# Performance work log

Hardware: AMD Instinct MI355X
Metric: run time of the kernel (lower is better)

Reference implementation:

```python
import jax, jax.numpy as jnp
import numpy as np

D_MODEL = 512
NUM_HEADS = 8
HEAD_DIM = D_MODEL // NUM_HEADS
BATCH = 4
SEQ = 2048
ROPE_BASE = 10000.0


def rope_cos_sin(seq_len, head_dim):
    inv_freq = 1.0 / (ROPE_BASE ** (jnp.arange(0, head_dim, 2, dtype=jnp.float32) / head_dim))
    t = jnp.arange(seq_len, dtype=jnp.float32)
    freqs = jnp.outer(t, inv_freq)              # (S, head_dim/2)
    emb = jnp.concatenate([freqs, freqs], axis=-1)  # (S, head_dim)
    return jnp.cos(emb), jnp.sin(emb)


def apply_rope(x, cos, sin):
    # x: (..., S, head_dim); cos/sin: (S, head_dim)
    x1 = x[..., ::2]
    x2 = x[..., 1::2]
    ch = cos[..., ::2]
    sh = sin[..., ::2]
    r1 = x1 * ch - x2 * sh
    r2 = x1 * sh + x2 * ch
    return jnp.stack([r1, r2], axis=-1).reshape(x.shape)


def setup_inputs() -> dict:
    key = jax.random.key(0)
    ks = jax.random.split(key, 12)
    x = jax.random.normal(ks[0], (BATCH, SEQ, D_MODEL), dtype=jnp.float32)
    variate_ids = jnp.sort(jax.random.randint(ks[1], (BATCH, SEQ), 0, 8), axis=-1).astype(jnp.int64)
    mask = jnp.ones((BATCH, SEQ), dtype=jnp.float32)
    s = 1.0 / np.sqrt(D_MODEL)
    Wq = jax.random.normal(ks[2], (D_MODEL, D_MODEL), dtype=jnp.float32) * s
    bq = jnp.zeros((D_MODEL,), dtype=jnp.float32)
    Wk = jax.random.normal(ks[3], (D_MODEL, D_MODEL), dtype=jnp.float32) * s
    bk = jnp.zeros((D_MODEL,), dtype=jnp.float32)
    Wv = jax.random.normal(ks[4], (D_MODEL, D_MODEL), dtype=jnp.float32) * s
    bv = jnp.zeros((D_MODEL,), dtype=jnp.float32)
    Wo = jax.random.normal(ks[5], (D_MODEL, D_MODEL), dtype=jnp.float32) * s
    bo = jnp.zeros((D_MODEL,), dtype=jnp.float32)
    u_same = jax.random.normal(ks[6], (NUM_HEADS,), dtype=jnp.float32) * 0.1
    u_cross = jax.random.normal(ks[7], (NUM_HEADS,), dtype=jnp.float32) * 0.1
    return dict(x=x, variate_ids=variate_ids, mask=mask, Wq=Wq, bq=bq, Wk=Wk, bk=bk,
                Wv=Wv, bv=bv, Wo=Wo, bo=bo, u_same=u_same, u_cross=u_cross)


def reference(x, variate_ids, mask, Wq, bq, Wk, bk, Wv, bv, Wo, bo, u_same, u_cross):
    B, S, D = x.shape
    H, Hd = NUM_HEADS, HEAD_DIM
    scale = 1.0 / np.sqrt(Hd)

    def proj(W, b):
        return (x @ W.T + b).reshape(B, S, H, Hd).transpose(0, 2, 1, 3)  # (B,H,S,Hd)

    q = proj(Wq, bq)
    k = proj(Wk, bk)
    v = proj(Wv, bv)

    cos, sin = rope_cos_sin(S, Hd)
    q = apply_rope(q, cos, sin)
    k = apply_rope(k, cos, sin)

    scores = jnp.einsum('bhid,bhjd->bhij', q, k) * scale  # (B,H,S,S)
    same = (variate_ids[:, :, None] == variate_ids[:, None, :]).astype(jnp.float32)  # (B,S,S)
    bias = same[:, None] * u_same[None, :, None, None] + (1.0 - same)[:, None] * u_cross[None, :, None, None]
    scores = scores + bias
    scores = scores + (1.0 - mask[:, None, None, :]) * -1e9
    probs = jax.nn.softmax(scores, axis=-1)
    out = jnp.einsum('bhij,bhjd->bhid', probs, v)  # (B,H,S,Hd)
    out = out.transpose(0, 2, 1, 3).reshape(B, S, D)
    return out @ Wo.T + bo
```

## Files before the change

kernel.cpp:

```cpp
#include <hip/hip_runtime.h>
#include <hip/hip_bf16.h>

#define BATCH   4
#define SEQ     2048
#define DMODEL  512
#define NHEADS  8
#define HEADDIM 64
#define MTOT    (BATCH*SEQ)
#define NX      (MTOT*DMODEL)
#define NW      (DMODEL*DMODEL)
#define QTILE   128
#define KTILE   64
#define NKT     (SEQ/KTILE)

#define LOG2E   1.4426950408889634f
#define SCL2    0.18033688011112042f
#define SHIFT   14.426950408889634f

typedef unsigned short u16;
typedef __bf16 bf16x8 __attribute__((ext_vector_type(8)));
typedef float  f32x4  __attribute__((ext_vector_type(4)));
typedef unsigned short u16x4 __attribute__((ext_vector_type(4)));
typedef unsigned u32x2 __attribute__((ext_vector_type(2)));

#define MFMA(a,b,c) __builtin_amdgcn_mfma_f32_16x16x32_bf16(a,b,c,0,0,0)

__device__ __forceinline__ u16 f2bf(float f) {
    unsigned u = __float_as_uint(f);
    u += 0x7FFFu + ((u >> 16) & 1u);
    return (u16)(u >> 16);
}
__device__ __forceinline__ unsigned pk_bf16(float a, float b) {
    union { __hip_bfloat162 h; unsigned u; } cv;
    cv.h = __float22bfloat162_rn(make_float2(a, b));
    return cv.u;
}
__device__ __forceinline__ float qsum16(float v) {
    v += __shfl_xor(v, 1);
    v += __shfl_xor(v, 2);
    v += __shfl_xor(v, 4);
    v += __shfl_xor(v, 8);
    return v;
}
__device__ __forceinline__ void gll16(const void* g, void* l) {
    __builtin_amdgcn_global_load_lds((const __attribute__((address_space(1))) void*)g,
                                     (__attribute__((address_space(3))) void*)l, 16, 0, 0);
}
__device__ __forceinline__ void gll4(const void* g, void* l) {
    __builtin_amdgcn_global_load_lds((const __attribute__((address_space(1))) void*)g,
                                     (__attribute__((address_space(3))) void*)l, 4, 0, 0);
}

#define NCVT4 ((NX + 4*NW)/4)
__global__ __launch_bounds__(256) void cvt_rope_kernel(
    const float* __restrict__ x,
    const float* __restrict__ wq, const float* __restrict__ wk,
    const float* __restrict__ wv, const float* __restrict__ wo,
    u16* __restrict__ xbf,
    u16* __restrict__ wqbf, u16* __restrict__ wkbf,
    u16* __restrict__ wvbf, u16* __restrict__ wobf,
    float2* __restrict__ cst)
{
    int i4 = blockIdx.x * 256 + threadIdx.x;
    if (i4 < NCVT4) {
        int i = i4 * 4;
        const float* s; u16* d; int o;
        if (i < NX) { s = x; d = xbf; o = i; }
        else {
            int j = i - NX;
            int r = j >> 18;
            o = j & (NW - 1);
            s = (r == 0) ? wq : (r == 1) ? wk : (r == 2) ? wv : wo;
            d = (r == 0) ? wqbf : (r == 1) ? wkbf : (r == 2) ? wvbf : wobf;
        }
        float4 v = *(const float4*)(s + o);
        u16x4 u = { f2bf(v.x), f2bf(v.y), f2bf(v.z), f2bf(v.w) };
        *(u16x4*)(d + o) = u;
    } else {
        int r = i4 - NCVT4;
        if (r < SEQ * 32 / 4) {
            int idx = r * 4;
            int s  = idx >> 5;
            int p0 = idx & 31;
#pragma unroll
            for (int t = 0; t < 4; ++t) {
                int p = p0 + t;
                float inv = __expf(-0.5756462732485115f * (float)(p & 15));
                float ang = (float)s * inv;
                cst[idx + t] = make_float2(cosf(ang), sinf(ang));
            }
        }
    }
}

#define TP 136
__global__ __launch_bounds__(256) void qkv_kernel(
    const u16* __restrict__ x,
    const u16* __restrict__ Wq, const float* __restrict__ bq,
    const u16* __restrict__ Wk, const float* __restrict__ bk,
    const u16* __restrict__ Wv, const float* __restrict__ bv,
    const float* __restrict__ cstf,
    u16* __restrict__ qws, u16* __restrict__ kws, u16* __restrict__ vtws)
{
    __shared__ alignas(16) u16 smem[128 * TP];
    u16* As = smem;
    u16* Bs = smem + 8192;

    const int m0 = blockIdx.x * 128;
    const int n0 = blockIdx.y * 128;
    const int tid  = threadIdx.x;
    const int w    = tid >> 6;
    const int lane = tid & 63;
    const int quad = lane >> 4;
    const int l16  = lane & 15;
    const int wm = w & 1, wn = w >> 1;

    const int sec = n0 >> 9;
    const int oc0 = n0 & 511;
    const u16*   Wm = (sec == 0) ? Wq : (sec == 1 ? Wk : Wv);
    const float* bb = (sec == 0) ? bq : (sec == 1 ? bk : bv);

    const int xb = (sec < 2) ? wn : wm;
    const int wb = (sec < 2) ? wm : wn;

    f32x4 acc[4][4] = {};

    for (int kb = 0; kb < 8; ++kb) {
#pragma unroll
        for (int it = 0; it < 4; ++it) {
            const int s   = it * 256 + tid;
            const int row = s >> 3;
            const int cb  = s & 7;
            const int gcol = kb * 64 + (((cb ^ (row & 7))) << 3);
            gll16(x  + (m0  + row) * 512 + gcol, &As[s * 8]);
            gll16(Wm + (oc0 + row) * 512 + gcol, &Bs[s * 8]);
        }
        __syncthreads();

#pragma unroll
        for (int ks = 0; ks < 2; ++ks) {
            bf16x8 xf[4], wf[4];
#pragma unroll
            for (int t = 0; t < 4; ++t) {
                const int xrow = xb * 64 + t * 16 + l16;
                const int wrow = wb * 64 + t * 16 + l16;
                xf[t] = *(const bf16x8*)&As[xrow * 64 + (((ks * 4 + quad) ^ (xrow & 7)) << 3)];
                wf[t] = *(const bf16x8*)&Bs[wrow * 64 + (((ks * 4 + quad) ^ (wrow & 7)) << 3)];
            }
            if (sec < 2) {
#pragma unroll
                for (int tm = 0; tm < 4; ++tm)
#pragma unroll
                    for (int tn = 0; tn < 4; ++tn)
                        acc[tm][tn] = MFMA(wf[tm], xf[tn], acc[tm][tn]);
            } else {
#pragma unroll
                for (int tm = 0; tm < 4; ++tm)
#pragma unroll
                    for (int tn = 0; tn < 4; ++tn)
                        acc[tm][tn] = MFMA(xf[tm], wf[tn], acc[tm][tn]);
            }
        }
        __syncthreads();
    }

    if (sec < 2) {
#pragma unroll
        for (int tm = 0; tm < 4; ++tm) {
            const int dls = wm * 64 + tm * 16 + quad * 4;
            const float4 bv4 = *(const float4*)&bb[oc0 + dls];
            const int pbase = ((oc0 + dls) & 63) >> 1;
#pragma unroll
            for (int tn = 0; tn < 4; ++tn) {
                const int sl = wn * 64 + tn * 16 + l16;
                const int sg = (m0 + sl) & 2047;
                const float4 cs = *(const float4*)&cstf[sg * 64 + pbase * 2];
                const float v0 = acc[tm][tn][0] + bv4.x;
                const float v1 = acc[tm][tn][1] + bv4.y;
                const float v2 = acc[tm][tn][2] + bv4.z;
                const float v3 = acc[tm][tn][3] + bv4.w;
                const float r0 = v0 * cs.x - v1 * cs.y;
                const float r1 = v1 * cs.x + v0 * cs.y;
                const float r2 = v2 * cs.z - v3 * cs.w;
                const float r3 = v3 * cs.z + v2 * cs.w;
                u32x2 pv = { pk_bf16(r0, r1), pk_bf16(r2, r3) };
                *(u32x2*)&smem[sl * TP + dls] = pv;
            }
        }
        __syncthreads();
        u16* dst0 = (sec == 0) ? qws : kws;
#pragma unroll
        for (int i = 0; i < 8; ++i) {
            const int c   = i * 256 + tid;
            const int sl  = c >> 4;
            const int d8  = (c & 15) * 8;
            const int gcol = oc0 + d8;
            const int hh  = gcol >> 6;
            const int dh  = gcol & 63;
            const int sgl = m0 + sl;
            const int bi  = sgl >> 11;
            const int s   = sgl & 2047;
            u16* dst = dst0 + (size_t)(bi * NHEADS + hh) * (SEQ * HEADDIM)
                            + (size_t)s * HEADDIM + dh;
            *(bf16x8*)dst = *(const bf16x8*)&smem[sl * TP + d8];
        }
    } else {
#pragma unroll
        for (int tm = 0; tm < 4; ++tm) {
            const int row_l = wm * 64 + tm * 16 + quad * 4;
#pragma unroll
            for (int tn = 0; tn < 4; ++tn) {
                const int col_l = wn * 64 + tn * 16 + l16;
                const float bval = bb[oc0 + col_l];
                u32x2 pv = { pk_bf16(acc[tm][tn][0] + bval, acc[tm][tn][1] + bval),
                             pk_bf16(acc[tm][tn][2] + bval, acc[tm][tn][3] + bval) };
                *(u32x2*)&smem[col_l * TP + row_l] = pv;
            }
        }
        __syncthreads();
        const int bi  = m0 >> 11;
        const int sgb = m0 & 2047;
#pragma unroll
        for (int i = 0; i < 8; ++i) {
            const int c    = i * 256 + tid;
            const int col  = c >> 4;
            const int sc8  = (c & 15) * 8;
            const int gcol = oc0 + col;
            const int hh   = gcol >> 6;
            const int d    = gcol & 63;
            u16* dst = vtws + (size_t)(bi * NHEADS + hh) * (SEQ * HEADDIM)
                            + (size_t)d * SEQ + sgb + sc8;
            *(bf16x8*)dst = *(const bf16x8*)&smem[col * TP + sc8];
        }
    }
}

__global__ __launch_bounds__(512, 4) void attn_kernel(
    const u16* __restrict__ qws, const u16* __restrict__ kws,
    const u16* __restrict__ vtl,
    const int* __restrict__ vids, const float* __restrict__ mask,
    const float* __restrict__ u_same, const float* __restrict__ u_cross,
    u16* __restrict__ attn)
{
    __shared__ alignas(16) u16 kbuf[2][KTILE * 64];
    __shared__ alignas(16) u16 vbuf[2][KTILE * 64];
    __shared__ alignas(16) u16 pls[8][16][72];
    __shared__ int   bid[2][KTILE];
    __shared__ float bmk[2][KTILE];

    const int bh = blockIdx.y;
    const int b  = bh >> 3;
    const int h  = bh & 7;
    const int q0 = blockIdx.x * QTILE;

    const int tid  = threadIdx.x;
    const int w    = tid >> 6;
    const int lane = tid & 63;
    const int quad = lane >> 4;
    const int l16  = lane & 15;

    const float us2 = u_same[h]  * LOG2E;
    const float uc2 = u_cross[h] * LOG2E;
    const size_t tb = (size_t)bh * (SEQ * HEADDIM);

    const int qr = q0 + w * 16 + l16;
    const bf16x8 aq0 = *(const bf16x8*)(qws + tb + qr * HEADDIM + quad * 8);
    const bf16x8 aq1 = *(const bf16x8*)(qws + tb + qr * HEADDIM + 32 + quad * 8);

    int vq[4];
#pragma unroll
    for (int r = 0; r < 4; ++r)
        vq[r] = vids[b * SEQ + q0 + w * 16 + quad * 4 + r];

    float li[4] = {0.f, 0.f, 0.f, 0.f};
    f32x4 o[4] = {};

    const int srow = w * 8 + (lane >> 3);
    const int scb  = lane & 7;
    const int soff = ((scb ^ (srow & 7)) << 3);
    auto stage = [&](int kt, int nb) {
        const int k0 = kt * KTILE;
        gll16(kws + tb + (size_t)(k0 + srow) * HEADDIM + soff, &kbuf[nb][w * 512 + lane * 8]);
        gll16(vtl + tb + (size_t)srow * SEQ + k0 + soff,       &vbuf[nb][w * 512 + lane * 8]);
        if (w == 0) {
            gll4(vids + b * SEQ + k0 + lane, &bid[nb][0]);
            gll4(mask + b * SEQ + k0 + lane, &bmk[nb][0]);
        }
    };

    auto body = [&](const int cur) {
#pragma unroll
        for (int nt = 0; nt < 4; ++nt) {
            const int krow = nt * 16 + l16;
            const int r7   = krow & 7;
            const bf16x8 kb0 = *(const bf16x8*)&kbuf[cur][krow * 64 + ((quad ^ r7) << 3)];
            const bf16x8 kb1 = *(const bf16x8*)&kbuf[cur][krow * 64 + ((quad ^ r7 ^ 4) << 3)];
            f32x4 sc = {};
            sc = MFMA(aq0, kb0, sc);
            sc = MFMA(aq1, kb1, sc);
            const int   kv  = bid[cur][krow];
            const float mdl = fmaf(bmk[cur][krow], 1.4426950408889634e9f,
                                   -1.4426950408889634e9f - SHIFT);
            const float as_ = us2 + mdl;
            const float ac_ = uc2 + mdl;
            float p[4];
#pragma unroll
            for (int r = 0; r < 4; ++r) {
                const float sel = (kv == vq[r]) ? as_ : ac_;
                p[r] = exp2f(fmaf(sc[r], SCL2, sel));
                li[r] += p[r];
            }
            const unsigned p01 = pk_bf16(p[0], p[1]);
            const unsigned p23 = pk_bf16(p[2], p[3]);
            u16* pb = &pls[w][quad * 4][nt * 16 + l16];
            pb[0]       = (u16)p01;  pb[72]      = (u16)(p01 >> 16);
            pb[2 * 72]  = (u16)p23;  pb[3 * 72]  = (u16)(p23 >> 16);
        }

        const bf16x8 ap0 = *(const bf16x8*)&pls[w][l16][quad * 8];
        const bf16x8 ap1 = *(const bf16x8*)&pls[w][l16][32 + quad * 8];

#pragma unroll
        for (int nt = 0; nt < 4; ++nt) {
            const int vrow = nt * 16 + l16;
            const int r7   = vrow & 7;
            const bf16x8 vb0 = *(const bf16x8*)&vbuf[cur][vrow * 64 + ((quad ^ r7) << 3)];
            const bf16x8 vb1 = *(const bf16x8*)&vbuf[cur][vrow * 64 + ((quad ^ r7 ^ 4) << 3)];
            o[nt] = MFMA(ap0, vb0, o[nt]);
            o[nt] = MFMA(ap1, vb1, o[nt]);
        }
    };

    stage(0, 0);
    for (int kt = 0; kt < NKT; kt += 2) {
        __syncthreads();
        stage(kt + 1, 1);
        body(0);
        __syncthreads();
        if (kt + 2 < NKT) stage(kt + 2, 0);
        body(1);
    }

#pragma unroll
    for (int r = 0; r < 4; ++r) {
        const float inv = 1.0f / qsum16(li[r]);
        const int R = q0 + w * 16 + quad * 4 + r;
        const int rb = (b * SEQ + R) * DMODEL + h * HEADDIM;
#pragma unroll
        for (int nt = 0; nt < 4; ++nt)
            attn[rb + nt * 16 + l16] = f2bf(o[nt][r] * inv);
    }
}

__global__ __launch_bounds__(256) void proj_kernel(
    const u16* __restrict__ a, const u16* __restrict__ Wo,
    const float* __restrict__ bo, float* __restrict__ out)
{
    __shared__ alignas(16) u16 psm[132 * 64 * 2];
    u16* As = psm;
    u16* Bs = psm + 8192;
    float* Lp = (float*)psm;

    const int m0 = blockIdx.x * 128;
    const int n0 = blockIdx.y * 128;
    const int tid  = threadIdx.x;
    const int w    = tid >> 6;
    const int lane = tid & 63;
    const int quad = lane >> 4;
    const int l16  = lane & 15;
    const int wm = w & 1, wn = w >> 1;

    f32x4 acc[4][4] = {};

    for (int kb = 0; kb < 8; ++kb) {
#pragma unroll
        for (int it = 0; it < 4; ++it) {
            const int s   = it * 256 + tid;
            const int row = s >> 3;
            const int cb  = s & 7;
            const int gcol = kb * 64 + (((cb ^ (row & 7))) << 3);
            gll16(a  + (m0 + row) * 512 + gcol, &As[s * 8]);
            gll16(Wo + (n0 + row) * 512 + gcol, &Bs[s * 8]);
        }
        __syncthreads();

#pragma unroll
        for (int ks = 0; ks < 2; ++ks) {
            bf16x8 af[4], wf[4];
#pragma unroll
            for (int t = 0; t < 4; ++t) {
                const int arow = wn * 64 + t * 16 + l16;
                const int wrow = wm * 64 + t * 16 + l16;
                af[t] = *(const bf16x8*)&As[arow * 64 + (((ks * 4 + quad) ^ (arow & 7)) << 3)];
                wf[t] = *(const bf16x8*)&Bs[wrow * 64 + (((ks * 4 + quad) ^ (wrow & 7)) << 3)];
            }
#pragma unroll
            for (int tm = 0; tm < 4; ++tm)
#pragma unroll
                for (int tn = 0; tn < 4; ++tn)
                    acc[tm][tn] = MFMA(wf[tm], af[tn], acc[tm][tn]);
        }
        __syncthreads();
    }

#pragma unroll
    for (int hph = 0; hph < 2; ++hph) {
        if (wn == hph) {
#pragma unroll
            for (int tm = 0; tm < 4; ++tm) {
                const int dls = wm * 64 + tm * 16 + quad * 4;
                const float4 bv4 = *(const float4*)&bo[n0 + dls];
#pragma unroll
                for (int tn = 0; tn < 4; ++tn) {
                    const int s2 = tn * 16 + l16;
                    float4 v = { acc[tm][tn][0] + bv4.x, acc[tm][tn][1] + bv4.y,
                                 acc[tm][tn][2] + bv4.z, acc[tm][tn][3] + bv4.w };
                    *(float4*)&Lp[s2 * 132 + dls] = v;
                }
            }
        }
        __syncthreads();
#pragma unroll
        for (int i = 0; i < 8; ++i) {
            const int c  = i * 256 + tid;
            const int s2 = c >> 5;
            const int dq = (c & 31) * 4;
            float4 v = *(const float4*)&Lp[s2 * 132 + dq];
            *(float4*)&out[(size_t)(m0 + hph * 64 + s2) * 512 + n0 + dq] = v;
        }
        __syncthreads();
    }
}

extern "C" void kernel_launch(void* const* d_in, const int* in_sizes, int n_in,
                              void* d_out, int out_size, void* d_ws, size_t ws_size,
                              hipStream_t stream) {
    const float* x    = (const float*)d_in[0];
    const int*   vids = (const int*)d_in[1];
    const float* mask = (const float*)d_in[2];
    const float* Wq = (const float*)d_in[3];
    const float* bq = (const float*)d_in[4];
    const float* Wk = (const float*)d_in[5];
    const float* bk = (const float*)d_in[6];
    const float* Wv = (const float*)d_in[7];
    const float* bv = (const float*)d_in[8];
    const float* Wo = (const float*)d_in[9];
    const float* bo = (const float*)d_in[10];
    const float* usame  = (const float*)d_in[11];
    const float* ucross = (const float*)d_in[12];
    float* out = (float*)d_out;

    u16* xbf  = (u16*)d_ws;
    u16* wqbf = xbf + NX;
    u16* wkbf = wqbf + NW;
    u16* wvbf = wkbf + NW;
    u16* wobf = wvbf + NW;
    float2* cst = (float2*)(wobf + NW);
    u16* qws  = (u16*)(cst + SEQ * 32);
    u16* kws  = qws + (size_t)BATCH * NHEADS * SEQ * HEADDIM;
    u16* vtws = kws + (size_t)BATCH * NHEADS * SEQ * HEADDIM;
    u16* attn = xbf;

    cvt_rope_kernel<<<(NCVT4 + SEQ * 32 / 4 + 255) / 256, 256, 0, stream>>>(
        x, Wq, Wk, Wv, Wo, xbf, wqbf, wkbf, wvbf, wobf, cst);

    dim3 g1(MTOT / 128, 3 * DMODEL / 128);
    qkv_kernel<<<g1, 256, 0, stream>>>(xbf, wqbf, bq, wkbf, bk, wvbf, bv,
                                       (const float*)cst, qws, kws, vtws);

    dim3 g2(SEQ / QTILE, BATCH * NHEADS);
    attn_kernel<<<g2, 512, 0, stream>>>(qws, kws, vtws, vids, mask,
                                        usame, ucross, attn);

    dim3 g3(MTOT / 128, DMODEL / 128);
    proj_kernel<<<g3, 256, 0, stream>>>(attn, wobf, bo, out);
}
```

Before: 205.6 us.

## Split attention KV range across two wave groups and reduce partials in LDS

The attention kernel now uses a 64-row query tile and splits the key sequence between two groups of four waves. Each group processes half the keys with 32-key tiles, and the partial outputs and row sums are combined through shared memory at the end. This doubles the number of blocks and raises the occupancy hint so more waves can hide latency. It also switches to the hardware exp2 builtin. The cost is an extra LDS reduction pass and smaller MFMA tiles per step, which means more loop overhead per key.

```diff
diff --git a/kernel.cpp b/kernel.cpp
--- a/kernel.cpp
+++ b/kernel.cpp
@@ -9,9 +9,9 @@
 #define MTOT    (BATCH*SEQ)
 #define NX      (MTOT*DMODEL)
 #define NW      (DMODEL*DMODEL)
-#define QTILE   128
-#define KTILE   64
-#define NKT     (SEQ/KTILE)
+#define QTILE   64
+#define KTILE   32
+#define NKT_G   32
 
 #define LOG2E   1.4426950408889634f
 #define SCL2    0.18033688011112042f
@@ -235,18 +235,17 @@
     }
 }
 
-__global__ __launch_bounds__(512, 4) void attn_kernel(
+__global__ __launch_bounds__(512, 6) void attn_kernel(
     const u16* __restrict__ qws, const u16* __restrict__ kws,
     const u16* __restrict__ vtl,
     const int* __restrict__ vids, const float* __restrict__ mask,
     const float* __restrict__ u_same, const float* __restrict__ u_cross,
     u16* __restrict__ attn)
 {
-    __shared__ alignas(16) u16 kbuf[2][KTILE * 64];
-    __shared__ alignas(16) u16 vbuf[2][KTILE * 64];
-    __shared__ alignas(16) u16 pls[8][16][72];
-    __shared__ int   bid[2][KTILE];
-    __shared__ float bmk[2][KTILE];
+    __shared__ alignas(16) u16 smem[21504];
+    __shared__ int   bidm[2][2][KTILE];
+    __shared__ float bmkm[2][2][KTILE];
+    __shared__ float comb_li[QTILE];
 
     const int bh = blockIdx.y;
     const int b  = bh >> 3;
@@ -258,48 +257,62 @@
     const int lane = tid & 63;
     const int quad = lane >> 4;
     const int l16  = lane & 15;
+    const int qw   = w & 3;
+    const int kg   = w >> 2;
+    const int tl   = tid & 255;
 
     const float us2 = u_same[h]  * LOG2E;
     const float uc2 = u_cross[h] * LOG2E;
     const size_t tb = (size_t)bh * (SEQ * HEADDIM);
 
-    const int qr = q0 + w * 16 + l16;
+    const int qr = q0 + qw * 16 + l16;
     const bf16x8 aq0 = *(const bf16x8*)(qws + tb + qr * HEADDIM + quad * 8);
     const bf16x8 aq1 = *(const bf16x8*)(qws + tb + qr * HEADDIM + 32 + quad * 8);
 
     int vq[4];
 #pragma unroll
     for (int r = 0; r < 4; ++r)
-        vq[r] = vids[b * SEQ + q0 + w * 16 + quad * 4 + r];
+        vq[r] = vids[b * SEQ + q0 + qw * 16 + quad * 4 + r];
 
     float li[4] = {0.f, 0.f, 0.f, 0.f};
     f32x4 o[4] = {};
 
-    const int srow = w * 8 + (lane >> 3);
-    const int scb  = lane & 7;
-    const int soff = ((scb ^ (srow & 7)) << 3);
-    auto stage = [&](int kt, int nb) {
-        const int k0 = kt * KTILE;
-        gll16(kws + tb + (size_t)(k0 + srow) * HEADDIM + soff, &kbuf[nb][w * 512 + lane * 8]);
-        gll16(vtl + tb + (size_t)srow * SEQ + k0 + soff,       &vbuf[nb][w * 512 + lane * 8]);
-        if (w == 0) {
-            gll4(vids + b * SEQ + k0 + lane, &bid[nb][0]);
-            gll4(mask + b * SEQ + k0 + lane, &bmk[nb][0]);
+    const int srow  = tl >> 3;
+    const int scb   = tl & 7;
+    const int soff  = ((scb ^ (srow & 7)) << 3);
+    const int vrow  = tl >> 2;
+    const int vcb   = tl & 3;
+    const int soffv = ((vcb ^ (vrow & 3)) << 3);
+    const int kbase = kg * 2 * 2048;
+
+    auto stage = [&](int t, int nb) {
+        const int k0 = (kg * NKT_G + t) * KTILE;
+        gll16(kws + tb + (size_t)(k0 + srow) * HEADDIM + soff,
+              &smem[kbase + nb * 2048 + tl * 8]);
+        gll16(vtl + tb + (size_t)vrow * SEQ + k0 + soffv,
+              &smem[8192 + kbase + nb * 2048 + tl * 8]);
+        if (tl < KTILE) {
+            gll4(vids + b * SEQ + k0 + tl, &bidm[kg][nb][0]);
+            gll4(mask + b * SEQ + k0 + tl, &bmkm[kg][nb][0]);
         }
     };
 
+    u16* const pls = &smem[16384 + w * 640];
+
     auto body = [&](const int cur) {
-#pragma unroll
-        for (int nt = 0; nt < 4; ++nt) {
+        const u16* kb_b = &smem[kbase + cur * 2048];
+        const u16* vb_b = &smem[8192 + kbase + cur * 2048];
+#pragma unroll
+        for (int nt = 0; nt < 2; ++nt) {
             const int krow = nt * 16 + l16;
             const int r7   = krow & 7;
-            const bf16x8 kb0 = *(const bf16x8*)&kbuf[cur][krow * 64 + ((quad ^ r7) << 3)];
-            const bf16x8 kb1 = *(const bf16x8*)&kbuf[cur][krow * 64 + ((quad ^ r7 ^ 4) << 3)];
+            const bf16x8 kb0 = *(const bf16x8*)&kb_b[krow * 64 + ((quad ^ r7) << 3)];
+            const bf16x8 kb1 = *(const bf16x8*)&kb_b[krow * 64 + ((quad ^ r7 ^ 4) << 3)];
             f32x4 sc = {};
             sc = MFMA(aq0, kb0, sc);
             sc = MFMA(aq1, kb1, sc);
-            const int   kv  = bid[cur][krow];
-            const float mdl = fmaf(bmk[cur][krow], 1.4426950408889634e9f,
+            const int   kv  = bidm[kg][cur][krow];
+            const float mdl = fmaf(bmkm[kg][cur][krow], 1.4426950408889634e9f,
                                    -1.4426950408889634e9f - SHIFT);
             const float as_ = us2 + mdl;
             const float ac_ = uc2 + mdl;
@@ -307,48 +320,64 @@
 #pragma unroll
             for (int r = 0; r < 4; ++r) {
                 const float sel = (kv == vq[r]) ? as_ : ac_;
-                p[r] = exp2f(fmaf(sc[r], SCL2, sel));
+                p[r] = __builtin_amdgcn_exp2f(fmaf(sc[r], SCL2, sel));
                 li[r] += p[r];
             }
             const unsigned p01 = pk_bf16(p[0], p[1]);
             const unsigned p23 = pk_bf16(p[2], p[3]);
-            u16* pb = &pls[w][quad * 4][nt * 16 + l16];
-            pb[0]       = (u16)p01;  pb[72]      = (u16)(p01 >> 16);
-            pb[2 * 72]  = (u16)p23;  pb[3 * 72]  = (u16)(p23 >> 16);
-        }
-
-        const bf16x8 ap0 = *(const bf16x8*)&pls[w][l16][quad * 8];
-        const bf16x8 ap1 = *(const bf16x8*)&pls[w][l16][32 + quad * 8];
+            u16* pb = &pls[(quad * 4) * 40 + nt * 16 + l16];
+            pb[0]   = (u16)p01;  pb[40]  = (u16)(p01 >> 16);
+            pb[80]  = (u16)p23;  pb[120] = (u16)(p23 >> 16);
+        }
+
+        const bf16x8 ap0 = *(const bf16x8*)&pls[l16 * 40 + quad * 8];
 
 #pragma unroll
         for (int nt = 0; nt < 4; ++nt) {
-            const int vrow = nt * 16 + l16;
-            const int r7   = vrow & 7;
-            const bf16x8 vb0 = *(const bf16x8*)&vbuf[cur][vrow * 64 + ((quad ^ r7) << 3)];
-            const bf16x8 vb1 = *(const bf16x8*)&vbuf[cur][vrow * 64 + ((quad ^ r7 ^ 4) << 3)];
+            const int vr = nt * 16 + l16;
+            const bf16x8 vb0 = *(const bf16x8*)&vb_b[vr * 32 + ((quad ^ (vr & 3)) << 3)];
             o[nt] = MFMA(ap0, vb0, o[nt]);
-            o[nt] = MFMA(ap1, vb1, o[nt]);
         }
     };
 
     stage(0, 0);
-    for (int kt = 0; kt < NKT; kt += 2) {
-        __syncthreads();
-        stage(kt + 1, 1);
+    for (int t = 0; t < NKT_G; t += 2) {
+        __syncthreads();
+        stage(t + 1, 1);
         body(0);
         __syncthreads();
-        if (kt + 2 < NKT) stage(kt + 2, 0);
+        if (t + 2 < NKT_G) stage(t + 2, 0);
         body(1);
     }
 
-#pragma unroll
-    for (int r = 0; r < 4; ++r) {
-        const float inv = 1.0f / qsum16(li[r]);
-        const int R = q0 + w * 16 + quad * 4 + r;
-        const int rb = (b * SEQ + R) * DMODEL + h * HEADDIM;
+    __syncthreads();
+    float* co = (float*)smem;
+    if (kg == 1) {
+#pragma unroll
+        for (int r = 0; r < 4; ++r) {
+            const float liq = qsum16(li[r]);
+            if (l16 == 0) comb_li[qw * 16 + quad * 4 + r] = liq;
+        }
 #pragma unroll
         for (int nt = 0; nt < 4; ++nt)
-            attn[rb + nt * 16 + l16] = f2bf(o[nt][r] * inv);
+#pragma unroll
+            for (int r = 0; r < 4; ++r)
+                co[(qw * 16 + quad * 4 + r) * 65 + nt * 16 + l16] = o[nt][r];
+    }
+    __syncthreads();
+    if (kg == 0) {
+#pragma unroll
+        for (int r = 0; r < 4; ++r) {
+            const int qloc = qw * 16 + quad * 4 + r;
+            const float lt = qsum16(li[r]) + comb_li[qloc];
+            const float inv = 1.0f / lt;
+            const int R  = q0 + qloc;
+            const int rb = (b * SEQ + R) * DMODEL + h * HEADDIM;
+#pragma unroll
+            for (int nt = 0; nt < 4; ++nt)
+                attn[rb + nt * 16 + l16] =
+                    f2bf((o[nt][r] + co[qloc * 65 + nt * 16 + l16]) * inv);
+        }
     }
 }
 
```

New measurement: 203.9 us. No clear change (-0.8%).
